# Optimization experiments

Measured on AMD Instinct MI355X. Metric: run time of the kernel, lower is better.

The kernel has to match this reference:

```python
import jax, jax.numpy as jnp
import numpy as np

KERNEL_SIZE = 11  # int(resolution / 11.6) with resolution=128
SIGMA = 1.5
K1, K2 = 0.01, 0.03


def gaussian_kernel(k=KERNEL_SIZE, sigma=SIGMA):
    coords = jnp.arange(k, dtype=jnp.float32) - (k - 1) / 2
    g = jnp.exp(-coords ** 2 / (2 * sigma ** 2))
    g = g / g.sum()
    return jnp.outer(g, g)  # (k,k)


def depthwise_conv(x, kern):
    # x: (N,C,H,W), kern: (k,k); depthwise (groups=C), SAME padding, stride 1
    C = x.shape[1]
    k = kern.shape[0]
    w = jnp.broadcast_to(kern[None, None], (C, 1, k, k))
    return jax.lax.conv_general_dilated(
        x, w, window_strides=(1, 1), padding='SAME',
        feature_group_count=C,
        dimension_numbers=('NCHW', 'OIHW', 'NCHW'))


def dssim_map(x, y, kern):
    C1, C2 = K1 ** 2, K2 ** 2
    mu_x = depthwise_conv(x, kern)
    mu_y = depthwise_conv(y, kern)
    sigma_x = depthwise_conv(x * x, kern) - mu_x ** 2
    sigma_y = depthwise_conv(y * y, kern) - mu_y ** 2
    sigma_xy = depthwise_conv(x * y, kern) - mu_x * mu_y
    ssim_num = (2 * mu_x * mu_y + C1) * (2 * sigma_xy + C2)
    ssim_den = (mu_x ** 2 + mu_y ** 2 + C1) * (sigma_x + sigma_y + C2)
    ssim = ssim_num / (ssim_den + 1e-8)
    return (1 - ssim) / 2  # (N,C,H,W)


def poly_mask(pts, H, W):
    # pts: (P,2) polygon vertices (x, y). Vectorized ray-casting point-in-polygon,
    # restricted to the truncated bounding box exactly like the torch code
    # (mask[:, :, ymin:ymax, xmin:xmax] slice), and zeroed if polygon exits frame.
    x, y = pts[:, 0], pts[:, 1]
    xmin, xmax = jnp.floor(x.min()), jnp.floor(x.max())  # == int() for positive coords
    ymin, ymax = jnp.floor(y.min()), jnp.floor(y.max())
    valid = (xmin >= 0) & (ymin >= 0) & (xmax < W) & (ymax < H)
    yy, xx = jnp.meshgrid(jnp.arange(H, dtype=jnp.float32),
                          jnp.arange(W, dtype=jnp.float32), indexing='ij')
    x1, y1 = x[:, None, None], y[:, None, None]        # (P,1,1)
    x2 = jnp.roll(x, -1)[:, None, None]
    y2 = jnp.roll(y, -1)[:, None, None]
    Y, X = yy[None], xx[None]                          # (1,H,W)
    cond = ((y1 > Y) != (y2 > Y)) & (X < (x2 - x1) * (Y - y1) / (y2 - y1 + 1e-6) + x1)
    inside = (cond.sum(axis=0) % 2) == 1               # XOR-fold over edges, (H,W)
    bbox = (yy >= ymin) & (yy < ymax) & (xx >= xmin) & (xx < xmax)
    return jnp.where(valid, (inside & bbox).astype(jnp.float32), 0.0)


def weight_map(lmrk, H, W):
    # lmrk: (68,2). weight = 1 + 3*eyeL + 3*eyeR + 2*mouth (additive, as in torch)
    return (1.0
            + 3.0 * poly_mask(lmrk[36:42], H, W)
            + 3.0 * poly_mask(lmrk[42:48], H, W)
            + 2.0 * poly_mask(lmrk[48:60], H, W))  # (H,W)


def setup_inputs() -> dict:
    key = jax.random.key(0)
    k1, k2, k3 = jax.random.split(key, 3)
    N, C, H, W = 48, 3, 256, 256
    pred = jax.random.normal(k1, (N, C, H, W), dtype=jnp.float32)
    target = jax.random.normal(k2, (N, C, H, W), dtype=jnp.float32)
    # landmarks strictly inside the frame so all polygons are rasterized
    landmarks = 20.0 + 216.0 * jax.random.uniform(k3, (N, 68, 2), dtype=jnp.float32)
    return {"pred": pred, "target": target, "landmarks": landmarks}


def reference(pred, target, landmarks):
    N, C, H, W = pred.shape
    kern = gaussian_kernel()
    # per-sample DSSIM (batch-of-1 conv in torch == batched conv here)
    d = dssim_map(pred, target, kern).mean(axis=(1, 2, 3))          # (N,)
    abs_diff = jnp.abs(pred - target)
    l1 = abs_diff.mean(axis=(1, 2, 3))                              # (N,)
    wmap = jax.vmap(lambda lm: weight_map(lm, H, W))(landmarks)     # (N,H,W)
    lw = (wmap[:, None] * abs_diff).mean(axis=(1, 2, 3))            # (N,)
    return (10.0 * d + 10.0 * l1 + 5.0 * lw).mean()
```

## Files before the change

kernel.cpp:

```cpp
#include <hip/hip_runtime.h>
#include <cmath>

#define HW 256
#define NIMG 48
#define NCH 3
#define NPLANE (NIMG * NCH)
#define STRIP 26
#define NSTRIP 10
#define NIN (STRIP + 10)
#define NCHUNK 4
#define NSLOT 64

__global__ void zero_ws_kernel(double* ws) {
    if (threadIdx.x < NSLOT) ws[threadIdx.x] = 0.0;
}

__launch_bounds__(256)
__global__ void fused_kernel(const float* __restrict__ pred,
                             const float* __restrict__ target,
                             const float* __restrict__ lmk,
                             double* __restrict__ ws)
{
    const int plane = blockIdx.x;
    const int n     = plane / 3;
    const int r0    = blockIdx.y * STRIP;
    const int x     = threadIdx.x;

    __shared__ float2 spt[11][HW + 10];
    __shared__ float  sxc[STRIP][24];
    __shared__ int    srowflag[STRIP];
    __shared__ float  slm[48];
    __shared__ float  sbbs[12];
    __shared__ float  svalids[3];
    __shared__ float  red[12];

    float g[11];
    {
        float gs = 0.f;
#pragma unroll
        for (int i = 0; i < 11; ++i) {
            float c = (float)i - 5.0f;
            g[i] = expf(-c * c / 4.5f);
            gs += g[i];
        }
#pragma unroll
        for (int i = 0; i < 11; ++i) g[i] /= gs;
    }

    if (x < 48) slm[x] = lmk[n * 136 + 72 + x];
    if (x < 5) {
#pragma unroll
        for (int t = 0; t < 11; ++t) {
            spt[t][x]       = make_float2(0.f, 0.f);
            spt[t][261 + x] = make_float2(0.f, 0.f);
        }
    }
    __syncthreads();

    if (x < 3) {
        const int s0 = (x == 0) ? 0 : (x == 1) ? 6 : 12;
        const int L  = (x == 2) ? 12 : 6;
        float xmn = 3e38f, xmx = -3e38f, ymn = 3e38f, ymx = -3e38f;
        for (int i = 0; i < L; ++i) {
            float px = slm[2 * (s0 + i)], py = slm[2 * (s0 + i) + 1];
            xmn = fminf(xmn, px); xmx = fmaxf(xmx, px);
            ymn = fminf(ymn, py); ymx = fmaxf(ymx, py);
        }
        xmn = floorf(xmn); xmx = floorf(xmx); ymn = floorf(ymn); ymx = floorf(ymx);
        sbbs[4 * x + 0] = xmn; sbbs[4 * x + 1] = xmx;
        sbbs[4 * x + 2] = ymn; sbbs[4 * x + 3] = ymx;
        svalids[x] = (xmn >= 0.f && ymn >= 0.f && xmx < 256.f && ymx < 256.f) ? 1.f : 0.f;
    }

#pragma unroll
    for (int u = 0; u < (STRIP * 24 + 255) / 256; ++u) {
        int idx = x + 256 * u;
        if (idx < STRIP * 24) {
            int r = idx / 24, e = idx - r * 24;
            float Y = (float)(r0 + r);
            const int s0 = (e < 6) ? 0 : (e < 12) ? 6 : 12;
            const int L  = (e < 12) ? 6 : 12;
            int il = e - s0;
            int i2 = (il + 1 == L) ? 0 : il + 1;
            float x1 = slm[2 * (s0 + il)], y1 = slm[2 * (s0 + il) + 1];
            float x2 = slm[2 * (s0 + i2)], y2 = slm[2 * (s0 + i2) + 1];
            bool crossing = (y1 > Y) != (y2 > Y);
            float xc = (x2 - x1) * (Y - y1) / (y2 - y1 + 1e-6f) + x1;
            sxc[r][e] = crossing ? xc : -3e38f;
        }
    }
    __syncthreads();

    if (x < STRIP) {
        float Y = (float)(r0 + x);
        int f = 0;
        if (svalids[0] != 0.f && Y >= sbbs[2]  && Y < sbbs[3])  f |= 1;
        if (svalids[1] != 0.f && Y >= sbbs[6]  && Y < sbbs[7])  f |= 2;
        if (svalids[2] != 0.f && Y >= sbbs[10] && Y < sbbs[11]) f |= 4;
        srowflag[x] = f;
    }
    __syncthreads();

    const float* __restrict__ pp = pred   + (size_t)plane * (HW * HW);
    const float* __restrict__ tp = target + (size_t)plane * (HW * HW);

    float ring[11][5];
#pragma unroll
    for (int s = 0; s < 11; ++s)
#pragma unroll
        for (int q = 0; q < 5; ++q) ring[s][q] = 0.f;

    float acc = 0.f, accl1 = 0.f, acclw = 0.f;
    const float X = (float)x;

    for (int c = 0; c < NCHUNK; ++c) {
        __syncthreads();
#pragma unroll
        for (int t = 0; t < 11; ++t) {
            int i = 11 * c + t;
            if (i < NIN) {
                int r_in = r0 - 5 + i;
                float pv = 0.f, tv = 0.f;
                if (r_in >= 0 && r_in < HW) {
                    pv = pp[r_in * HW + x];
                    tv = tp[r_in * HW + x];
                }
                spt[t][x + 5] = make_float2(pv, tv);
            }
        }
        __syncthreads();

#pragma unroll
        for (int t = 0; t < 11; ++t) {
            const int i = 11 * c + t;
            if (i >= NIN) continue;
            const int r_in = r0 - 5 + i;

            float h0 = 0.f, h1 = 0.f, h2 = 0.f, h3 = 0.f, h4 = 0.f;
            float2 center;
#pragma unroll
            for (int k = 0; k < 11; ++k) {
                float2 v = spt[t][x + k];
                if (k == 5) center = v;
                float w = g[k];
                float wp = w * v.x, wt = w * v.y;
                h0 += wp;
                h1 += wt;
                h2 = fmaf(wp, v.x, h2);
                h3 = fmaf(wt, v.y, h3);
                h4 = fmaf(wp, v.y, h4);
            }
            ring[t][0] = h0; ring[t][1] = h1; ring[t][2] = h2;
            ring[t][3] = h3; ring[t][4] = h4;

            if (i >= 5 && i < 5 + STRIP && r_in < HW) {
                float ad = fabsf(center.x - center.y);
                accl1 += ad;
                float wgt = 1.f;
                const int flags = srowflag[i - 5];
                if (flags) {
                    const float* xc = sxc[i - 5];
                    int c0 = 0, c1 = 0, c2 = 0;
#pragma unroll
                    for (int e = 0; e < 6; ++e)   c0 += (X < xc[e]) ? 1 : 0;
#pragma unroll
                    for (int e = 6; e < 12; ++e)  c1 += (X < xc[e]) ? 1 : 0;
#pragma unroll
                    for (int e = 12; e < 24; ++e) c2 += (X < xc[e]) ? 1 : 0;
                    if ((flags & 1) && (c0 & 1) && X >= sbbs[0] && X < sbbs[1]) wgt += 3.f;
                    if ((flags & 2) && (c1 & 1) && X >= sbbs[4] && X < sbbs[5]) wgt += 3.f;
                    if ((flags & 4) && (c2 & 1) && X >= sbbs[8] && X < sbbs[9]) wgt += 2.f;
                }
                acclw += wgt * ad;
            }

            if (i >= 10 && i < 10 + STRIP) {
                const int r_out = r0 + (i - 10);
                if (r_out < HW) {
                    float mux = 0.f, muy = 0.f, exx = 0.f, eyy = 0.f, exy = 0.f;
#pragma unroll
                    for (int j = 0; j < 11; ++j) {
                        const int s = (t + 1 + j) % 11;
                        float w = g[j];
                        mux = fmaf(w, ring[s][0], mux);
                        muy = fmaf(w, ring[s][1], muy);
                        exx = fmaf(w, ring[s][2], exx);
                        eyy = fmaf(w, ring[s][3], eyy);
                        exy = fmaf(w, ring[s][4], exy);
                    }
                    float sx  = exx - mux * mux;
                    float sy  = eyy - muy * muy;
                    float sxy = exy - mux * muy;
                    const float C1 = 1e-4f, C2 = 9e-4f;
                    float num = (2.f * mux * muy + C1) * (2.f * sxy + C2);
                    float den = (mux * mux + muy * muy + C1) * (sx + sy + C2);
                    acc += 0.5f * (1.f - num / (den + 1e-8f));
                }
            }
        }
    }

#pragma unroll
    for (int off = 32; off > 0; off >>= 1) {
        acc   += __shfl_down(acc, off, 64);
        accl1 += __shfl_down(accl1, off, 64);
        acclw += __shfl_down(acclw, off, 64);
    }
    if ((x & 63) == 0) {
        int w = x >> 6;
        red[w] = acc; red[4 + w] = accl1; red[8 + w] = acclw;
    }
    __syncthreads();
    if (x == 0) {
        double s = 10.0 * ((double)red[0] + red[1] + red[2]  + red[3])
                 + 10.0 * ((double)red[4] + red[5] + red[6]  + red[7])
                 +  5.0 * ((double)red[8] + red[9] + red[10] + red[11]);
        atomicAdd(&ws[(blockIdx.y * NPLANE + blockIdx.x) & (NSLOT - 1)], s);
    }
}

__global__ void final_kernel(const double* __restrict__ ws, float* __restrict__ out) {
    double v = ws[threadIdx.x];
#pragma unroll
    for (int off = 32; off > 0; off >>= 1)
        v += __shfl_down(v, off, 64);
    if (threadIdx.x == 0) {
        const double denom = (double)NIMG * NCH * HW * HW;
        out[0] = (float)(v / denom);
    }
}

extern "C" void kernel_launch(void* const* d_in, const int* in_sizes, int n_in,
                              void* d_out, int out_size, void* d_ws, size_t ws_size,
                              hipStream_t stream)
{
    const float* pred   = (const float*)d_in[0];
    const float* target = (const float*)d_in[1];
    const float* lmk    = (const float*)d_in[2];
    float* out  = (float*)d_out;
    double* ws  = (double*)d_ws;

    hipLaunchKernelGGL(zero_ws_kernel, dim3(1), dim3(64), 0, stream, ws);
    hipLaunchKernelGGL(fused_kernel, dim3(NPLANE, NSTRIP), dim3(256), 0, stream,
                       pred, target, lmk, ws);
    hipLaunchKernelGGL(final_kernel, dim3(1), dim3(64), 0, stream, ws, out);
}
```

Baseline: 169.6 us.

## Split image columns into two 128-wide tiles and enlarge row strips

```diff
diff --git a/kernel.cpp b/kernel.cpp
--- a/kernel.cpp
+++ b/kernel.cpp
@@ -5,17 +5,19 @@
 #define NIMG 48
 #define NCH 3
 #define NPLANE (NIMG * NCH)
-#define STRIP 26
-#define NSTRIP 10
+#define STRIP 37
+#define NSTRIP 7
+#define COLS 128
+#define NCB 2
 #define NIN (STRIP + 10)
-#define NCHUNK 4
+#define NCHUNK 5
 #define NSLOT 64
 
 __global__ void zero_ws_kernel(double* ws) {
     if (threadIdx.x < NSLOT) ws[threadIdx.x] = 0.0;
 }
 
-__launch_bounds__(256)
+__launch_bounds__(128)
 __global__ void fused_kernel(const float* __restrict__ pred,
                              const float* __restrict__ target,
                              const float* __restrict__ lmk,
@@ -24,15 +26,15 @@
     const int plane = blockIdx.x;
     const int n     = plane / 3;
     const int r0    = blockIdx.y * STRIP;
+    const int c0    = blockIdx.z * COLS;
     const int x     = threadIdx.x;
 
-    __shared__ float2 spt[11][HW + 10];
+    __shared__ float2 spt[11][COLS + 10];
     __shared__ float  sxc[STRIP][24];
     __shared__ int    srowflag[STRIP];
     __shared__ float  slm[48];
     __shared__ float  sbbs[12];
     __shared__ float  svalids[3];
-    __shared__ float  red[12];
 
     float g[11];
     {
@@ -48,13 +50,6 @@
     }
 
     if (x < 48) slm[x] = lmk[n * 136 + 72 + x];
-    if (x < 5) {
-#pragma unroll
-        for (int t = 0; t < 11; ++t) {
-            spt[t][x]       = make_float2(0.f, 0.f);
-            spt[t][261 + x] = make_float2(0.f, 0.f);
-        }
-    }
     __syncthreads();
 
     if (x < 3) {
@@ -73,8 +68,8 @@
     }
 
 #pragma unroll
-    for (int u = 0; u < (STRIP * 24 + 255) / 256; ++u) {
-        int idx = x + 256 * u;
+    for (int u = 0; u < (STRIP * 24 + 127) / 128; ++u) {
+        int idx = x + 128 * u;
         if (idx < STRIP * 24) {
             int r = idx / 24, e = idx - r * 24;
             float Y = (float)(r0 + r);
@@ -111,7 +106,7 @@
         for (int q = 0; q < 5; ++q) ring[s][q] = 0.f;
 
     float acc = 0.f, accl1 = 0.f, acclw = 0.f;
-    const float X = (float)x;
+    const float X = (float)(c0 + x);
 
     for (int c = 0; c < NCHUNK; ++c) {
         __syncthreads();
@@ -120,12 +115,24 @@
             int i = 11 * c + t;
             if (i < NIN) {
                 int r_in = r0 - 5 + i;
-                float pv = 0.f, tv = 0.f;
-                if (r_in >= 0 && r_in < HW) {
-                    pv = pp[r_in * HW + x];
-                    tv = tp[r_in * HW + x];
-                }
-                spt[t][x + 5] = make_float2(pv, tv);
+                {
+                    int gc = c0 - 5 + x;
+                    float pv = 0.f, tv = 0.f;
+                    if (r_in >= 0 && r_in < HW && gc >= 0) {
+                        pv = pp[r_in * HW + gc];
+                        tv = tp[r_in * HW + gc];
+                    }
+                    spt[t][x] = make_float2(pv, tv);
+                }
+                if (x < 10) {
+                    int gc = c0 + 123 + x;
+                    float pv = 0.f, tv = 0.f;
+                    if (r_in >= 0 && r_in < HW && gc < HW) {
+                        pv = pp[r_in * HW + gc];
+                        tv = tp[r_in * HW + gc];
+                    }
+                    spt[t][COLS + x] = make_float2(pv, tv);
+                }
             }
         }
         __syncthreads();
@@ -160,16 +167,16 @@
                 const int flags = srowflag[i - 5];
                 if (flags) {
                     const float* xc = sxc[i - 5];
-                    int c0 = 0, c1 = 0, c2 = 0;
-#pragma unroll
-                    for (int e = 0; e < 6; ++e)   c0 += (X < xc[e]) ? 1 : 0;
-#pragma unroll
-                    for (int e = 6; e < 12; ++e)  c1 += (X < xc[e]) ? 1 : 0;
-#pragma unroll
-                    for (int e = 12; e < 24; ++e) c2 += (X < xc[e]) ? 1 : 0;
-                    if ((flags & 1) && (c0 & 1) && X >= sbbs[0] && X < sbbs[1]) wgt += 3.f;
-                    if ((flags & 2) && (c1 & 1) && X >= sbbs[4] && X < sbbs[5]) wgt += 3.f;
-                    if ((flags & 4) && (c2 & 1) && X >= sbbs[8] && X < sbbs[9]) wgt += 2.f;
+                    int c0c = 0, c1c = 0, c2c = 0;
+#pragma unroll
+                    for (int e = 0; e < 6; ++e)   c0c += (X < xc[e]) ? 1 : 0;
+#pragma unroll
+                    for (int e = 6; e < 12; ++e)  c1c += (X < xc[e]) ? 1 : 0;
+#pragma unroll
+                    for (int e = 12; e < 24; ++e) c2c += (X < xc[e]) ? 1 : 0;
+                    if ((flags & 1) && (c0c & 1) && X >= sbbs[0] && X < sbbs[1]) wgt += 3.f;
+                    if ((flags & 2) && (c1c & 1) && X >= sbbs[4] && X < sbbs[5]) wgt += 3.f;
+                    if ((flags & 4) && (c2c & 1) && X >= sbbs[8] && X < sbbs[9]) wgt += 2.f;
                 }
                 acclw += wgt * ad;
             }
@@ -207,15 +214,9 @@
         acclw += __shfl_down(acclw, off, 64);
     }
     if ((x & 63) == 0) {
-        int w = x >> 6;
-        red[w] = acc; red[4 + w] = accl1; red[8 + w] = acclw;
-    }
-    __syncthreads();
-    if (x == 0) {
-        double s = 10.0 * ((double)red[0] + red[1] + red[2]  + red[3])
-                 + 10.0 * ((double)red[4] + red[5] + red[6]  + red[7])
-                 +  5.0 * ((double)red[8] + red[9] + red[10] + red[11]);
-        atomicAdd(&ws[(blockIdx.y * NPLANE + blockIdx.x) & (NSLOT - 1)], s);
+        double s = 10.0 * (double)acc + 10.0 * (double)accl1 + 5.0 * (double)acclw;
+        int bid = (blockIdx.z * NSTRIP + blockIdx.y) * NPLANE + blockIdx.x;
+        atomicAdd(&ws[(2 * bid + (x >> 6)) & (NSLOT - 1)], s);
     }
 }
 
@@ -241,7 +242,7 @@
     double* ws  = (double*)d_ws;
 
     hipLaunchKernelGGL(zero_ws_kernel, dim3(1), dim3(64), 0, stream, ws);
-    hipLaunchKernelGGL(fused_kernel, dim3(NPLANE, NSTRIP), dim3(256), 0, stream,
+    hipLaunchKernelGGL(fused_kernel, dim3(NPLANE, NSTRIP, NCB), dim3(128), 0, stream,
                        pred, target, lmk, ws);
     hipLaunchKernelGGL(final_kernel, dim3(1), dim3(64), 0, stream, ws, out);
 }
```

After: 162.7 us. 1.04x faster.

## Reorder separable SSIM to vertical-first with register ring and double-buffered LDS

Applied to the files above, without the earlier changes.

```diff
diff --git a/kernel.cpp b/kernel.cpp
--- a/kernel.cpp
+++ b/kernel.cpp
@@ -5,10 +5,11 @@
 #define NIMG 48
 #define NCH 3
 #define NPLANE (NIMG * NCH)
-#define STRIP 26
-#define NSTRIP 10
+#define STRIP 37
+#define NSTRIP 7
 #define NIN (STRIP + 10)
-#define NCHUNK 4
+#define CHUNK 22
+#define NCHUNK 3
 #define NSLOT 64
 
 __global__ void zero_ws_kernel(double* ws) {
@@ -26,7 +27,8 @@
     const int r0    = blockIdx.y * STRIP;
     const int x     = threadIdx.x;
 
-    __shared__ float2 spt[11][HW + 10];
+    __shared__ float4 mva[2][HW + 10];
+    __shared__ float  mvb[2][HW + 10];
     __shared__ float  sxc[STRIP][24];
     __shared__ int    srowflag[STRIP];
     __shared__ float  slm[48];
@@ -34,26 +36,27 @@
     __shared__ float  svalids[3];
     __shared__ float  red[12];
 
-    float g[11];
+    float g6[6];
     {
-        float gs = 0.f;
-#pragma unroll
-        for (int i = 0; i < 11; ++i) {
-            float c = (float)i - 5.0f;
-            g[i] = expf(-c * c / 4.5f);
-            gs += g[i];
-        }
-#pragma unroll
-        for (int i = 0; i < 11; ++i) g[i] /= gs;
-    }
+        float gg[11]; float gs = 0.f;
+#pragma unroll
+        for (int q = 0; q < 11; ++q) {
+            float c = (float)q - 5.0f;
+            gg[q] = expf(-c * c / 4.5f);
+            gs += gg[q];
+        }
+#pragma unroll
+        for (int q = 0; q < 6; ++q) g6[q] = gg[q] / gs;
+    }
+#define GW(j) g6[(j) < 6 ? (j) : 10 - (j)]
 
     if (x < 48) slm[x] = lmk[n * 136 + 72 + x];
     if (x < 5) {
-#pragma unroll
-        for (int t = 0; t < 11; ++t) {
-            spt[t][x]       = make_float2(0.f, 0.f);
-            spt[t][261 + x] = make_float2(0.f, 0.f);
-        }
+        const float4 z4 = make_float4(0.f, 0.f, 0.f, 0.f);
+        mva[0][x] = z4; mva[0][261 + x] = z4;
+        mva[1][x] = z4; mva[1][261 + x] = z4;
+        mvb[0][x] = 0.f; mvb[0][261 + x] = 0.f;
+        mvb[1][x] = 0.f; mvb[1][261 + x] = 0.f;
     }
     __syncthreads();
 
@@ -61,8 +64,8 @@
         const int s0 = (x == 0) ? 0 : (x == 1) ? 6 : 12;
         const int L  = (x == 2) ? 12 : 6;
         float xmn = 3e38f, xmx = -3e38f, ymn = 3e38f, ymx = -3e38f;
-        for (int i = 0; i < L; ++i) {
-            float px = slm[2 * (s0 + i)], py = slm[2 * (s0 + i) + 1];
+        for (int q = 0; q < L; ++q) {
+            float px = slm[2 * (s0 + q)], py = slm[2 * (s0 + q) + 1];
             xmn = fminf(xmn, px); xmx = fmaxf(xmx, px);
             ymn = fminf(ymn, py); ymx = fmaxf(ymx, py);
         }
@@ -101,102 +104,119 @@
     }
     __syncthreads();
 
-    const float* __restrict__ pp = pred   + (size_t)plane * (HW * HW);
-    const float* __restrict__ tp = target + (size_t)plane * (HW * HW);
-
-    float ring[11][5];
-#pragma unroll
-    for (int s = 0; s < 11; ++s)
-#pragma unroll
-        for (int q = 0; q < 5; ++q) ring[s][q] = 0.f;
+    const float* __restrict__ pp = pred   + (size_t)plane * (HW * HW) + x;
+    const float* __restrict__ tp = target + (size_t)plane * (HW * HW) + x;
+
+    float rp[11], rt[11];
+    float pfap, pfat, pfbp, pfbt;
+    {
+        int ra = r0 - 5;
+        bool va = (ra >= 0);
+        pfap = va ? pp[(size_t)ra * HW] : 0.f;
+        pfat = va ? tp[(size_t)ra * HW] : 0.f;
+        int rb = r0 - 4;
+        bool vb = (rb >= 0);
+        pfbp = vb ? pp[(size_t)rb * HW] : 0.f;
+        pfbt = vb ? tp[(size_t)rb * HW] : 0.f;
+    }
 
     float acc = 0.f, accl1 = 0.f, acclw = 0.f;
     const float X = (float)x;
 
     for (int c = 0; c < NCHUNK; ++c) {
-        __syncthreads();
-#pragma unroll
-        for (int t = 0; t < 11; ++t) {
-            int i = 11 * c + t;
+#pragma unroll
+        for (int t = 0; t < CHUNK; ++t) {
+            const int i  = CHUNK * c + t;
+            const int sr = t % 11;
+
             if (i < NIN) {
-                int r_in = r0 - 5 + i;
-                float pv = 0.f, tv = 0.f;
-                if (r_in >= 0 && r_in < HW) {
-                    pv = pp[r_in * HW + x];
-                    tv = tp[r_in * HW + x];
-                }
-                spt[t][x + 5] = make_float2(pv, tv);
+                if ((t & 1) == 0) { rp[sr] = pfap; rt[sr] = pfat; }
+                else              { rp[sr] = pfbp; rt[sr] = pfbt; }
+                {
+                    int rin2 = r0 - 3 + i;
+                    bool v = (i + 2 < NIN) && (rin2 >= 0) && (rin2 < HW);
+                    float lp = 0.f, lt = 0.f;
+                    if (v) {
+                        lp = pp[(size_t)rin2 * HW];
+                        lt = tp[(size_t)rin2 * HW];
+                    }
+                    if ((t & 1) == 0) { pfap = lp; pfat = lt; }
+                    else              { pfbp = lp; pfbt = lt; }
+                }
+
+                if (i >= 5 && i < 5 + STRIP) {
+                    int r_in = r0 - 5 + i;
+                    if (r_in < HW) {
+                        float ad = fabsf(rp[sr] - rt[sr]);
+                        accl1 += ad;
+                        float wgt = 1.f;
+                        const int flags = srowflag[i - 5];
+                        if (flags) {
+                            const float* xc = sxc[i - 5];
+                            int c0 = 0, c1 = 0, c2 = 0;
+#pragma unroll
+                            for (int e = 0; e < 6; ++e)   c0 += (X < xc[e]) ? 1 : 0;
+#pragma unroll
+                            for (int e = 6; e < 12; ++e)  c1 += (X < xc[e]) ? 1 : 0;
+#pragma unroll
+                            for (int e = 12; e < 24; ++e) c2 += (X < xc[e]) ? 1 : 0;
+                            if ((flags & 1) && (c0 & 1) && X >= sbbs[0] && X < sbbs[1]) wgt += 3.f;
+                            if ((flags & 2) && (c1 & 1) && X >= sbbs[4] && X < sbbs[5]) wgt += 3.f;
+                            if ((flags & 4) && (c2 & 1) && X >= sbbs[8] && X < sbbs[9]) wgt += 2.f;
+                        }
+                        acclw += wgt * ad;
+                    }
+                }
             }
-        }
-        __syncthreads();
-
-#pragma unroll
-        for (int t = 0; t < 11; ++t) {
-            const int i = 11 * c + t;
-            if (i >= NIN) continue;
-            const int r_in = r0 - 5 + i;
-
-            float h0 = 0.f, h1 = 0.f, h2 = 0.f, h3 = 0.f, h4 = 0.f;
-            float2 center;
-#pragma unroll
-            for (int k = 0; k < 11; ++k) {
-                float2 v = spt[t][x + k];
-                if (k == 5) center = v;
-                float w = g[k];
-                float wp = w * v.x, wt = w * v.y;
-                h0 += wp;
-                h1 += wt;
-                h2 = fmaf(wp, v.x, h2);
-                h3 = fmaf(wt, v.y, h3);
-                h4 = fmaf(wp, v.y, h4);
-            }
-            ring[t][0] = h0; ring[t][1] = h1; ring[t][2] = h2;
-            ring[t][3] = h3; ring[t][4] = h4;
-
-            if (i >= 5 && i < 5 + STRIP && r_in < HW) {
-                float ad = fabsf(center.x - center.y);
-                accl1 += ad;
-                float wgt = 1.f;
-                const int flags = srowflag[i - 5];
-                if (flags) {
-                    const float* xc = sxc[i - 5];
-                    int c0 = 0, c1 = 0, c2 = 0;
-#pragma unroll
-                    for (int e = 0; e < 6; ++e)   c0 += (X < xc[e]) ? 1 : 0;
-#pragma unroll
-                    for (int e = 6; e < 12; ++e)  c1 += (X < xc[e]) ? 1 : 0;
-#pragma unroll
-                    for (int e = 12; e < 24; ++e) c2 += (X < xc[e]) ? 1 : 0;
-                    if ((flags & 1) && (c0 & 1) && X >= sbbs[0] && X < sbbs[1]) wgt += 3.f;
-                    if ((flags & 2) && (c1 & 1) && X >= sbbs[4] && X < sbbs[5]) wgt += 3.f;
-                    if ((flags & 4) && (c2 & 1) && X >= sbbs[8] && X < sbbs[9]) wgt += 2.f;
-                }
-                acclw += wgt * ad;
-            }
 
             if (i >= 10 && i < 10 + STRIP) {
-                const int r_out = r0 + (i - 10);
-                if (r_out < HW) {
+                int r = r0 + i - 10;
+                if (r < HW) {
                     float mux = 0.f, muy = 0.f, exx = 0.f, eyy = 0.f, exy = 0.f;
 #pragma unroll
                     for (int j = 0; j < 11; ++j) {
                         const int s = (t + 1 + j) % 11;
-                        float w = g[j];
-                        mux = fmaf(w, ring[s][0], mux);
-                        muy = fmaf(w, ring[s][1], muy);
-                        exx = fmaf(w, ring[s][2], exx);
-                        eyy = fmaf(w, ring[s][3], eyy);
-                        exy = fmaf(w, ring[s][4], exy);
-                    }
-                    float sx  = exx - mux * mux;
-                    float sy  = eyy - muy * muy;
-                    float sxy = exy - mux * muy;
+                        float w = GW(j);
+                        float p = rp[s], q = rt[s];
+                        float wp = w * p, wt = w * q;
+                        mux += wp; muy += wt;
+                        exx = fmaf(wp, p, exx);
+                        eyy = fmaf(wt, q, eyy);
+                        exy = fmaf(wp, q, exy);
+                    }
+                    mva[t & 1][x + 5] = make_float4(mux, muy, exx, eyy);
+                    mvb[t & 1][x + 5] = exy;
+                }
+            }
+
+            if (i >= 11 && i < 11 + STRIP) {
+                int rr = r0 + i - 11;
+                if (rr < HW) {
+                    const int b = (t + 1) & 1;
+                    float Mx = 0.f, My = 0.f, Exx = 0.f, Eyy = 0.f, Exy = 0.f;
+#pragma unroll
+                    for (int k = 0; k < 11; ++k) {
+                        float w = GW(k);
+                        float4 m4 = mva[b][x + k];
+                        float  m1 = mvb[b][x + k];
+                        Mx  = fmaf(w, m4.x, Mx);
+                        My  = fmaf(w, m4.y, My);
+                        Exx = fmaf(w, m4.z, Exx);
+                        Eyy = fmaf(w, m4.w, Eyy);
+                        Exy = fmaf(w, m1,  Exy);
+                    }
+                    float sx  = Exx - Mx * Mx;
+                    float sy  = Eyy - My * My;
+                    float sxy = Exy - Mx * My;
                     const float C1 = 1e-4f, C2 = 9e-4f;
-                    float num = (2.f * mux * muy + C1) * (2.f * sxy + C2);
-                    float den = (mux * mux + muy * muy + C1) * (sx + sy + C2);
+                    float num = (2.f * Mx * My + C1) * (2.f * sxy + C2);
+                    float den = (Mx * Mx + My * My + C1) * (sx + sy + C2);
                     acc += 0.5f * (1.f - num / (den + 1e-8f));
                 }
             }
+
+            asm volatile("s_waitcnt lgkmcnt(0)" ::: "memory");
+            __builtin_amdgcn_s_barrier();
         }
     }
 
```

Measured after the change: 153.0 us. 1.11x faster.
